# Kernel tuning notes

Hardware: AMD Instinct MI355X
Metric: run time of the kernel (lower is better)

Reference implementation:

```python
import jax, jax.numpy as jnp
import numpy as np

N_NODES = 50000
N_EDGES = 800000
IN_DIM = 128
HID = 128
BN_EPS = 1e-5


def _linear_init(key, fan_in, fan_out):
    kw, kb = jax.random.split(key)
    bound = 1.0 / np.sqrt(fan_in)
    w = jax.random.uniform(kw, (fan_in, fan_out), minval=-bound, maxval=bound, dtype=jnp.float32)
    b = jax.random.uniform(kb, (fan_out,), minval=-bound, maxval=bound, dtype=jnp.float32)
    return w, b


def setup_inputs() -> dict:
    key = jax.random.key(0)
    ks = jax.random.split(key, 8)
    x = jax.random.normal(ks[0], (N_NODES, IN_DIM), dtype=jnp.float32)
    edge_index = jax.random.randint(ks[1], (2, N_EDGES), 0, N_NODES, dtype=jnp.int32)
    # GIN layer 0 MLP: Linear(IN_DIM,HID) -> ReLU -> Linear(HID,HID)
    w0a, b0a = _linear_init(ks[2], IN_DIM, HID)
    w0b, b0b = _linear_init(ks[3], HID, HID)
    # GIN layer 1 MLP
    w1a, b1a = _linear_init(ks[4], HID, HID)
    w1b, b1b = _linear_init(ks[5], HID, HID)
    # encoder BatchNorm affine params (torch init: gamma=1, beta=0)
    bn_gamma = jnp.ones((HID,), jnp.float32)
    bn_beta = jnp.zeros((HID,), jnp.float32)
    # projection head: Linear(HID,HID) -> BatchNorm -> PReLU -> Dropout
    pw, pb = _linear_init(ks[6], HID, HID)
    pbn_gamma = jnp.ones((HID,), jnp.float32)
    pbn_beta = jnp.zeros((HID,), jnp.float32)
    prelu_a = jnp.asarray(0.25, jnp.float32)  # torch PReLU default init
    return {
        'x': x, 'edge_index': edge_index,
        'w0a': w0a, 'b0a': b0a, 'w0b': w0b, 'b0b': b0b,
        'w1a': w1a, 'b1a': b1a, 'w1b': w1b, 'b1b': b1b,
        'bn_gamma': bn_gamma, 'bn_beta': bn_beta,
        'pw': pw, 'pb': pb, 'pbn_gamma': pbn_gamma, 'pbn_beta': pbn_beta,
        'prelu_a': prelu_a,
    }


def _batch_norm(x, gamma, beta):
    # training-mode BatchNorm1d: biased variance over the node (batch) dim
    mu = jnp.mean(x, axis=0)
    var = jnp.var(x, axis=0)
    return gamma * (x - mu) * jax.lax.rsqrt(var + BN_EPS) + beta


def _gin_conv(z, src, dst, wa, ba, wb, bb):
    # sum-aggregate neighbor features: out[i] = (1+eps)*z[i] + sum_{j->i} z[j], eps=0
    agg = jax.ops.segment_sum(z[src], dst, num_segments=N_NODES)
    h = z + agg
    h = jax.nn.relu(h @ wa + ba)
    return h @ wb + bb


def reference(x, edge_index, w0a, b0a, w0b, b0b, w1a, b1a, w1b, b1b,
              bn_gamma, bn_beta, pw, pb, pbn_gamma, pbn_beta, prelu_a):
    src, dst = edge_index[0], edge_index[1]
    z = x
    z = jax.nn.relu(_gin_conv(z, src, dst, w0a, b0a, w0b, b0b))  # dropout: identity (deterministic)
    z = jax.nn.relu(_gin_conv(z, src, dst, w1a, b1a, w1b, b1b))
    z = _batch_norm(z, bn_gamma, bn_beta)
    p = z @ pw + pb
    p = _batch_norm(p, pbn_gamma, pbn_beta)
    p = jnp.where(p > 0, p, prelu_a * p)  # PReLU, single shared parameter
    return z, p
```

## Files before the change

kernel.cpp:

```cpp
#include <hip/hip_runtime.h>
#include <hip/hip_bf16.h>

#define NN 50000
#define NE 800000
#define HD 128
#define BN_EPS 1e-5f
#define MSTR 132
#define NBUK 782
#define PB 200
#define CHUNK 4000

typedef __attribute__((ext_vector_type(8))) __bf16 bf16x8;
typedef __attribute__((ext_vector_type(4))) __bf16 bf16x4;
typedef __attribute__((ext_vector_type(4))) float floatx4;

__global__ void k_zero_i(int* __restrict__ p, int n) {
    const int i = blockIdx.x * 256 + threadIdx.x;
    if (i < n) p[i] = 0;
}

__global__ __launch_bounds__(256) void k_cast(const float* __restrict__ X,
                                              __bf16* __restrict__ Y) {
    const int i8 = (blockIdx.x * 256 + threadIdx.x) * 8;
    const float4 a = *(const float4*)&X[i8];
    const float4 b = *(const float4*)&X[i8 + 4];
    bf16x8 o;
    o[0] = (__bf16)a.x; o[1] = (__bf16)a.y; o[2] = (__bf16)a.z; o[3] = (__bf16)a.w;
    o[4] = (__bf16)b.x; o[5] = (__bf16)b.y; o[6] = (__bf16)b.z; o[7] = (__bf16)b.w;
    *(bf16x8*)&Y[i8] = o;
}

__global__ void k_wprep(const float* __restrict__ W0, const float* __restrict__ W1,
                        const float* __restrict__ W2, const float* __restrict__ W3,
                        const float* __restrict__ W4,
                        __bf16* __restrict__ Bh, __bf16* __restrict__ Bl) {
    const int n = blockIdx.x, m = blockIdx.y, k = threadIdx.x;
    const float* W = (m == 0) ? W0 : (m == 1) ? W1 : (m == 2) ? W2 : (m == 3) ? W3 : W4;
    const float w = W[k * HD + n];
    const __bf16 h = (__bf16)w;
    const int ct = n >> 4, lm = n & 15;
    const int ks = k >> 5, lq = (k & 31) >> 3, j = k & 7;
    const int lane = lq * 16 + lm;
    const size_t o = (size_t)m * HD * HD + (size_t)(((ct * 4 + ks) * 64) + lane) * 8 + j;
    Bh[o] = h;
    Bl[o] = (__bf16)(w - (float)h);
}

__global__ __launch_bounds__(256) void k_bcount(const int* __restrict__ dst,
                                                int* __restrict__ gbtot) {
    __shared__ int h[NBUK];
    for (int i = threadIdx.x; i < NBUK; i += 256) h[i] = 0;
    __syncthreads();
    const int e0 = blockIdx.x * CHUNK;
    for (int i = threadIdx.x; i < CHUNK; i += 256)
        atomicAdd(&h[dst[e0 + i] >> 6], 1);
    __syncthreads();
    for (int i = threadIdx.x; i < NBUK; i += 256) {
        const int v = h[i];
        if (v) atomicAdd(&gbtot[i], v);
    }
}

__global__ __launch_bounds__(256) void k_bscan(const int* __restrict__ gbtot,
                                               int* __restrict__ bbase,
                                               int* __restrict__ gcur,
                                               int* __restrict__ rowptr) {
    __shared__ int sh[256];
    const int t = threadIdx.x;
    int v[4];
    int s = 0;
#pragma unroll
    for (int j = 0; j < 4; ++j) {
        const int idx = t * 4 + j;
        v[j] = (idx < NBUK) ? gbtot[idx] : 0;
        s += v[j];
    }
    sh[t] = s;
    __syncthreads();
#pragma unroll
    for (int st = 1; st < 256; st <<= 1) {
        int add = (t >= st) ? sh[t - st] : 0;
        __syncthreads();
        sh[t] += add;
        __syncthreads();
    }
    int run = sh[t] - s;
#pragma unroll
    for (int j = 0; j < 4; ++j) {
        const int idx = t * 4 + j;
        if (idx < NBUK) { bbase[idx] = run; gcur[idx] = run; }
        run += v[j];
    }
    if (t == 255) bbase[NBUK] = run;
    if (t == 0) rowptr[NN] = NE;
}

__global__ __launch_bounds__(256) void k_bscatter(const int* __restrict__ src,
                                                  const int* __restrict__ dst,
                                                  int* __restrict__ gcur,
                                                  int2* __restrict__ pairs) {
    __shared__ int h[NBUK];
    __shared__ int cur[NBUK];
    for (int i = threadIdx.x; i < NBUK; i += 256) h[i] = 0;
    __syncthreads();
    const int e0 = blockIdx.x * CHUNK;
    for (int i = threadIdx.x; i < CHUNK; i += 256)
        atomicAdd(&h[dst[e0 + i] >> 6], 1);
    __syncthreads();
    for (int i = threadIdx.x; i < NBUK; i += 256) {
        const int v = h[i];
        if (v) cur[i] = atomicAdd(&gcur[i], v);
    }
    __syncthreads();
    for (int i = threadIdx.x; i < CHUNK; i += 256) {
        const int d = dst[e0 + i];
        const int pos = atomicAdd(&cur[d >> 6], 1);
        pairs[pos] = make_int2(src[e0 + i], d);
    }
}

__global__ __launch_bounds__(256) void k_csrfin(const int2* __restrict__ pairs,
                                                const int* __restrict__ bbase,
                                                int* __restrict__ rowptr,
                                                int* __restrict__ esrc) {
    __shared__ int cnt[64], lof[64], cur[64];
    const int b = blockIdx.x;
    const int s = bbase[b], e = bbase[b + 1];
    const int tid = threadIdx.x;
    if (tid < 64) cnt[tid] = 0;
    __syncthreads();
    for (int i = s + tid; i < e; i += 256)
        atomicAdd(&cnt[pairs[i].y & 63], 1);
    __syncthreads();
    if (tid == 0) {
        int r = 0;
#pragma unroll
        for (int j = 0; j < 64; ++j) { lof[j] = r; cur[j] = r; r += cnt[j]; }
    }
    __syncthreads();
    if (tid < 64) {
        const int node = b * 64 + tid;
        if (node < NN) rowptr[node] = s + lof[tid];
    }
    for (int i = s + tid; i < e; i += 256) {
        const int2 p = pairs[i];
        const int pos = atomicAdd(&cur[p.y & 63], 1);
        esrc[s + pos] = p.x;
    }
}

__device__ __forceinline__ void split8(const float4 a, const float4 b,
                                       bf16x8& hi, bf16x8& lo) {
    hi[0] = (__bf16)a.x; lo[0] = (__bf16)(a.x - (float)hi[0]);
    hi[1] = (__bf16)a.y; lo[1] = (__bf16)(a.y - (float)hi[1]);
    hi[2] = (__bf16)a.z; lo[2] = (__bf16)(a.z - (float)hi[2]);
    hi[3] = (__bf16)a.w; lo[3] = (__bf16)(a.w - (float)hi[3]);
    hi[4] = (__bf16)b.x; lo[4] = (__bf16)(b.x - (float)hi[4]);
    hi[5] = (__bf16)b.y; lo[5] = (__bf16)(b.y - (float)hi[5]);
    hi[6] = (__bf16)b.z; lo[6] = (__bf16)(b.z - (float)hi[6]);
    hi[7] = (__bf16)b.w; lo[7] = (__bf16)(b.w - (float)hi[7]);
}

__device__ __forceinline__ void addb8(float4& a, float4& b, const bf16x8 v) {
    a.x += (float)v[0]; a.y += (float)v[1]; a.z += (float)v[2]; a.w += (float)v[3];
    b.x += (float)v[4]; b.y += (float)v[5]; b.z += (float)v[6]; b.w += (float)v[7];
}

__global__ __launch_bounds__(256) void k_aggb(const __bf16* __restrict__ Z,
                                              const int* __restrict__ rowptr,
                                              const int* __restrict__ esrc,
                                              float* __restrict__ H) {
    const int g = threadIdx.x >> 4;
    const int lg = threadIdx.x & 15;
    const int node = blockIdx.x * 16 + g;
    const int cb = lg * 8;
    const int start = rowptr[node], end = rowptr[node + 1];
    float4 a = {0.f, 0.f, 0.f, 0.f}, b = {0.f, 0.f, 0.f, 0.f};
    addb8(a, b, *(const bf16x8*)&Z[(size_t)node * HD + cb]);
    int k = start;
    for (; k + 8 <= end; k += 8) {
        const int s0 = esrc[k + 0], s1 = esrc[k + 1];
        const int s2 = esrc[k + 2], s3 = esrc[k + 3];
        const int s4 = esrc[k + 4], s5 = esrc[k + 5];
        const int s6 = esrc[k + 6], s7 = esrc[k + 7];
        const bf16x8 v0 = *(const bf16x8*)&Z[(size_t)s0 * HD + cb];
        const bf16x8 v1 = *(const bf16x8*)&Z[(size_t)s1 * HD + cb];
        const bf16x8 v2 = *(const bf16x8*)&Z[(size_t)s2 * HD + cb];
        const bf16x8 v3 = *(const bf16x8*)&Z[(size_t)s3 * HD + cb];
        const bf16x8 v4 = *(const bf16x8*)&Z[(size_t)s4 * HD + cb];
        const bf16x8 v5 = *(const bf16x8*)&Z[(size_t)s5 * HD + cb];
        const bf16x8 v6 = *(const bf16x8*)&Z[(size_t)s6 * HD + cb];
        const bf16x8 v7 = *(const bf16x8*)&Z[(size_t)s7 * HD + cb];
        addb8(a, b, v0); addb8(a, b, v1); addb8(a, b, v2); addb8(a, b, v3);
        addb8(a, b, v4); addb8(a, b, v5); addb8(a, b, v6); addb8(a, b, v7);
    }
    for (; k + 4 <= end; k += 4) {
        const int s0 = esrc[k + 0], s1 = esrc[k + 1];
        const int s2 = esrc[k + 2], s3 = esrc[k + 3];
        const bf16x8 v0 = *(const bf16x8*)&Z[(size_t)s0 * HD + cb];
        const bf16x8 v1 = *(const bf16x8*)&Z[(size_t)s1 * HD + cb];
        const bf16x8 v2 = *(const bf16x8*)&Z[(size_t)s2 * HD + cb];
        const bf16x8 v3 = *(const bf16x8*)&Z[(size_t)s3 * HD + cb];
        addb8(a, b, v0); addb8(a, b, v1); addb8(a, b, v2); addb8(a, b, v3);
    }
    for (; k < end; ++k) {
        const int s = esrc[k];
        addb8(a, b, *(const bf16x8*)&Z[(size_t)s * HD + cb]);
    }
    *(float4*)&H[(size_t)node * HD + cb] = a;
    *(float4*)&H[(size_t)node * HD + cb + 4] = b;
}

__device__ __forceinline__ void mfma_pass(floatx4 (&acc)[8], const bf16x8 ah,
                                          const bf16x8 al, const __bf16* Bh,
                                          const __bf16* Bl, int ks, int lane) {
#pragma unroll
    for (int ct = 0; ct < 8; ++ct) {
        const size_t bo = (size_t)(((ct * 4 + ks) * 64) + lane) * 8;
        const bf16x8 bh = *(const bf16x8*)&Bh[bo];
        const bf16x8 bl = *(const bf16x8*)&Bl[bo];
        acc[ct] = __builtin_amdgcn_mfma_f32_16x16x32_bf16(al, bh, acc[ct], 0, 0, 0);
        acc[ct] = __builtin_amdgcn_mfma_f32_16x16x32_bf16(ah, bl, acc[ct], 0, 0, 0);
        acc[ct] = __builtin_amdgcn_mfma_f32_16x16x32_bf16(ah, bh, acc[ct], 0, 0, 0);
    }
}

template <int STATS, int OUT16>
__global__ __launch_bounds__(256) void k_mlp(const float* __restrict__ A,
                                             const __bf16* __restrict__ Bh1,
                                             const __bf16* __restrict__ Bl1,
                                             const float* __restrict__ b1,
                                             const __bf16* __restrict__ Bh2,
                                             const __bf16* __restrict__ Bl2,
                                             const float* __restrict__ b2,
                                             float* __restrict__ C,
                                             __bf16* __restrict__ C16,
                                             float* __restrict__ pstat) {
    __shared__ float mid[4][16 * MSTR];
    __shared__ float ssum[128], ssq[128];
    const int tid = threadIdx.x;
    const int wid = tid >> 6, lane = tid & 63;
    const int lq = lane >> 4, lm = lane & 15;
    if (STATS) {
        if (tid < 128) { ssum[tid] = 0.f; ssq[tid] = 0.f; }
        __syncthreads();
    }
    const int rowbase = blockIdx.x * 64 + wid * 16;
    const int r0 = min(rowbase + lm, NN - 1);
    float* m = &mid[wid][0];

    floatx4 acc[8];
#pragma unroll
    for (int j = 0; j < 8; ++j) acc[j] = (floatx4){0.f, 0.f, 0.f, 0.f};
#pragma unroll
    for (int ks = 0; ks < 4; ++ks) {
        const int kk = ks * 32 + lq * 8;
        const float4 aa = *(const float4*)&A[(size_t)r0 * HD + kk];
        const float4 ab = *(const float4*)&A[(size_t)r0 * HD + kk + 4];
        bf16x8 ah, al;
        split8(aa, ab, ah, al);
        mfma_pass(acc, ah, al, Bh1, Bl1, ks, lane);
    }
#pragma unroll
    for (int ct = 0; ct < 8; ++ct) {
        const int col = ct * 16 + lm;
        const float bcol = b1[col];
#pragma unroll
        for (int r = 0; r < 4; ++r)
            m[(lq * 4 + r) * MSTR + col] = fmaxf(acc[ct][r] + bcol, 0.f);
    }
#pragma unroll
    for (int j = 0; j < 8; ++j) acc[j] = (floatx4){0.f, 0.f, 0.f, 0.f};
#pragma unroll
    for (int ks = 0; ks < 4; ++ks) {
        const int kk = ks * 32 + lq * 8;
        const float4 aa = *(const float4*)&m[lm * MSTR + kk];
        const float4 ab = *(const float4*)&m[lm * MSTR + kk + 4];
        bf16x8 ah, al;
        split8(aa, ab, ah, al);
        mfma_pass(acc, ah, al, Bh2, Bl2, ks, lane);
    }
#pragma unroll
    for (int ct = 0; ct < 8; ++ct) {
        const int col = ct * 16 + lm;
        const float bcol = b2[col];
#pragma unroll
        for (int r = 0; r < 4; ++r)
            m[(lq * 4 + r) * MSTR + col] = fmaxf(acc[ct][r] + bcol, 0.f);
    }
    float s0 = 0.f, s1 = 0.f, s2 = 0.f, s3 = 0.f;
    float q0 = 0.f, q1 = 0.f, q2 = 0.f, q3 = 0.f;
    const int c0 = (lane * 4) & 127;
#pragma unroll
    for (int p = 0; p < 8; ++p) {
        const int idx = p * 256 + lane * 4;
        const int r = idx >> 7;
        const float4 v = *(const float4*)&m[r * MSTR + c0];
        const int row = rowbase + r;
        if (row < NN) {
            if (OUT16) {
                bf16x4 o;
                o[0] = (__bf16)v.x; o[1] = (__bf16)v.y;
                o[2] = (__bf16)v.z; o[3] = (__bf16)v.w;
                *(bf16x4*)&C16[(size_t)row * HD + c0] = o;
            } else {
                *(float4*)&C[(size_t)row * HD + c0] = v;
            }
            if (STATS) {
                s0 += v.x; q0 = fmaf(v.x, v.x, q0);
                s1 += v.y; q1 = fmaf(v.y, v.y, q1);
                s2 += v.z; q2 = fmaf(v.z, v.z, q2);
                s3 += v.w; q3 = fmaf(v.w, v.w, q3);
            }
        }
    }
    if (STATS) {
        s0 += __shfl_xor(s0, 32); q0 += __shfl_xor(q0, 32);
        s1 += __shfl_xor(s1, 32); q1 += __shfl_xor(q1, 32);
        s2 += __shfl_xor(s2, 32); q2 += __shfl_xor(q2, 32);
        s3 += __shfl_xor(s3, 32); q3 += __shfl_xor(q3, 32);
        if (lane < 32) {
            atomicAdd(&ssum[c0 + 0], s0); atomicAdd(&ssq[c0 + 0], q0);
            atomicAdd(&ssum[c0 + 1], s1); atomicAdd(&ssq[c0 + 1], q1);
            atomicAdd(&ssum[c0 + 2], s2); atomicAdd(&ssq[c0 + 2], q2);
            atomicAdd(&ssum[c0 + 3], s3); atomicAdd(&ssq[c0 + 3], q3);
        }
        __syncthreads();
        if (tid < 128) {
            pstat[(size_t)blockIdx.x * 256 + tid] = ssum[tid];
            pstat[(size_t)blockIdx.x * 256 + 128 + tid] = ssq[tid];
        }
    }
}

__global__ __launch_bounds__(256) void k_proj(const float* __restrict__ Z2,
                                              const float* __restrict__ bnsc,
                                              const float* __restrict__ bnsh,
                                              float* __restrict__ Zout,
                                              const __bf16* __restrict__ Bh,
                                              const __bf16* __restrict__ Bl,
                                              const float* __restrict__ bias,
                                              float* __restrict__ C,
                                              float* __restrict__ pstat) {
    __shared__ float tb[4][16 * MSTR];
    __shared__ float ssum[128], ssq[128];
    const int tid = threadIdx.x;
    const int wid = tid >> 6, lane = tid & 63;
    const int lq = lane >> 4, lm = lane & 15;
    if (tid < 128) { ssum[tid] = 0.f; ssq[tid] = 0.f; }
    __syncthreads();
    const int rowbase = blockIdx.x * 64 + wid * 16;
    const int r0 = min(rowbase + lm, NN - 1);
    const bool rowok = (rowbase + lm) < NN;
    float* m = &tb[wid][0];

    floatx4 acc[8];
#pragma unroll
    for (int j = 0; j < 8; ++j) acc[j] = (floatx4){0.f, 0.f, 0.f, 0.f};
#pragma unroll
    for (int ks = 0; ks < 4; ++ks) {
        const int kk = ks * 32 + lq * 8;
        const float4 za = *(const float4*)&Z2[(size_t)r0 * HD + kk];
        const float4 zb = *(const float4*)&Z2[(size_t)r0 * HD + kk + 4];
        const float4 sca = *(const float4*)&bnsc[kk];
        const float4 scb = *(const float4*)&bnsc[kk + 4];
        const float4 sha = *(const float4*)&bnsh[kk];
        const float4 shb = *(const float4*)&bnsh[kk + 4];
        float4 aa, ab;
        aa.x = fmaf(za.x, sca.x, sha.x); aa.y = fmaf(za.y, sca.y, sha.y);
        aa.z = fmaf(za.z, sca.z, sha.z); aa.w = fmaf(za.w, sca.w, sha.w);
        ab.x = fmaf(zb.x, scb.x, shb.x); ab.y = fmaf(zb.y, scb.y, shb.y);
        ab.z = fmaf(zb.z, scb.z, shb.z); ab.w = fmaf(zb.w, scb.w, shb.w);
        if (rowok) {
            *(float4*)&Zout[(size_t)r0 * HD + kk] = aa;
            *(float4*)&Zout[(size_t)r0 * HD + kk + 4] = ab;
        }
        bf16x8 ah, al;
        split8(aa, ab, ah, al);
        mfma_pass(acc, ah, al, Bh, Bl, ks, lane);
    }
#pragma unroll
    for (int ct = 0; ct < 8; ++ct) {
        const int col = ct * 16 + lm;
        const float bcol = bias[col];
#pragma unroll
        for (int r = 0; r < 4; ++r)
            m[(lq * 4 + r) * MSTR + col] = acc[ct][r] + bcol;
    }
    float s0 = 0.f, s1 = 0.f, s2 = 0.f, s3 = 0.f;
    float q0 = 0.f, q1 = 0.f, q2 = 0.f, q3 = 0.f;
    const int c0 = (lane * 4) & 127;
#pragma unroll
    for (int p = 0; p < 8; ++p) {
        const int idx = p * 256 + lane * 4;
        const int r = idx >> 7;
        const float4 v = *(const float4*)&m[r * MSTR + c0];
        const int row = rowbase + r;
        if (row < NN) {
            *(float4*)&C[(size_t)row * HD + c0] = v;
            s0 += v.x; q0 = fmaf(v.x, v.x, q0);
            s1 += v.y; q1 = fmaf(v.y, v.y, q1);
            s2 += v.z; q2 = fmaf(v.z, v.z, q2);
            s3 += v.w; q3 = fmaf(v.w, v.w, q3);
        }
    }
    s0 += __shfl_xor(s0, 32); q0 += __shfl_xor(q0, 32);
    s1 += __shfl_xor(s1, 32); q1 += __shfl_xor(q1, 32);
    s2 += __shfl_xor(s2, 32); q2 += __shfl_xor(q2, 32);
    s3 += __shfl_xor(s3, 32); q3 += __shfl_xor(q3, 32);
    if (lane < 32) {
        atomicAdd(&ssum[c0 + 0], s0); atomicAdd(&ssq[c0 + 0], q0);
        atomicAdd(&ssum[c0 + 1], s1); atomicAdd(&ssq[c0 + 1], q1);
        atomicAdd(&ssum[c0 + 2], s2); atomicAdd(&ssq[c0 + 2], q2);
        atomicAdd(&ssum[c0 + 3], s3); atomicAdd(&ssq[c0 + 3], q3);
    }
    __syncthreads();
    if (tid < 128) {
        pstat[(size_t)blockIdx.x * 256 + tid] = ssum[tid];
        pstat[(size_t)blockIdx.x * 256 + 128 + tid] = ssq[tid];
    }
}

__global__ __launch_bounds__(256) void k_sred(const float* __restrict__ ps, int nblk,
                                              float* __restrict__ out) {
    const int j = threadIdx.x;
    float acc = 0.f;
    for (int r = blockIdx.x; r < nblk; r += 64)
        acc += ps[(size_t)r * 256 + j];
    out[blockIdx.x * 256 + j] = acc;
}

__global__ void k_bnfin(const float* __restrict__ pb2,
                        const float* __restrict__ gamma, const float* __restrict__ beta,
                        float* __restrict__ scale, float* __restrict__ shift) {
    const int c = threadIdx.x;
    float s = 0.f, q = 0.f;
    for (int b = 0; b < 64; ++b) {
        s += pb2[b * 256 + c];
        q += pb2[b * 256 + 128 + c];
    }
    const float mean = s * (1.f / NN);
    const float var = q * (1.f / NN) - mean * mean;
    const float sc = gamma[c] * rsqrtf(var + BN_EPS);
    scale[c] = sc;
    shift[c] = beta[c] - mean * sc;
}

__global__ void k_bnapply(const float* __restrict__ X, const float* __restrict__ scale,
                          const float* __restrict__ shift, float* __restrict__ Y,
                          const float* __restrict__ pa) {
    const int i4 = (blockIdx.x * 256 + threadIdx.x) * 4;
    const int c = i4 & 127;
    const float4 sc = *(const float4*)&scale[c];
    const float4 sh = *(const float4*)&shift[c];
    const float4 v = *(const float4*)&X[i4];
    float4 y;
    y.x = fmaf(v.x, sc.x, sh.x);
    y.y = fmaf(v.y, sc.y, sh.y);
    y.z = fmaf(v.z, sc.z, sh.z);
    y.w = fmaf(v.w, sc.w, sh.w);
    const float a = pa[0];
    if (y.x < 0.f) y.x *= a;
    if (y.y < 0.f) y.y *= a;
    if (y.z < 0.f) y.z *= a;
    if (y.w < 0.f) y.w *= a;
    *(float4*)&Y[i4] = y;
}

extern "C" void kernel_launch(void* const* d_in, const int* in_sizes, int n_in,
                              void* d_out, int out_size, void* d_ws, size_t ws_size,
                              hipStream_t stream) {
    const float* x = (const float*)d_in[0];
    const int* ei = (const int*)d_in[1];
    const float* w0a = (const float*)d_in[2];
    const float* b0a = (const float*)d_in[3];
    const float* w0b = (const float*)d_in[4];
    const float* b0b = (const float*)d_in[5];
    const float* w1a = (const float*)d_in[6];
    const float* b1a = (const float*)d_in[7];
    const float* w1b = (const float*)d_in[8];
    const float* b1b = (const float*)d_in[9];
    const float* bng = (const float*)d_in[10];
    const float* bnb = (const float*)d_in[11];
    const float* pw  = (const float*)d_in[12];
    const float* pb  = (const float*)d_in[13];
    const float* pbng = (const float*)d_in[14];
    const float* pbnb = (const float*)d_in[15];
    const float* pa = (const float*)d_in[16];

    float* outZ = (float*)d_out;
    float* outP = outZ + (size_t)NN * HD;

    float* ws = (float*)d_ws;
    float* bufH = ws;
    float* st = bufH + (size_t)NN * HD;
    int* rowptr = (int*)(st + 1024);
    int* esrc = rowptr + NN + 64;
    int* gbtot = esrc + NE;
    int* bbase = gbtot + 800;
    int* gcur = bbase + 800;
    __bf16* wth = (__bf16*)(gcur + 800);
    __bf16* wtl = wth + 5 * HD * HD;
    float* ps1 = (float*)(wtl + 5 * HD * HD);
    float* pb2a = ps1 + 800 * 256;
    float* ps2 = pb2a + 64 * 256;
    float* pb2b = ps2 + 800 * 256;

    __bf16* xb  = (__bf16*)bufH;
    __bf16* z1b = xb + (size_t)NN * HD;
    int2* pairs = (int2*)z1b;
    float* Hbuf = outP;

    const int* srcv = ei;
    const int* dstv = ei + NE;

    const int ELV = (NN * HD) / (256 * 4);
    const int CVB = (NN * HD) / (256 * 8);
    const int GB = (NN + 63) / 64;
    const int AB = NN / 16;

    k_wprep<<<dim3(HD, 5), HD, 0, stream>>>(w0a, w0b, w1a, w1b, pw, wth, wtl);
    k_cast<<<CVB, 256, 0, stream>>>(x, xb);
    k_zero_i<<<4, 256, 0, stream>>>(gbtot, 800);

    k_bcount<<<PB, 256, 0, stream>>>(dstv, gbtot);
    k_bscan<<<1, 256, 0, stream>>>(gbtot, bbase, gcur, rowptr);
    k_bscatter<<<PB, 256, 0, stream>>>(srcv, dstv, gcur, pairs);
    k_csrfin<<<NBUK, 256, 0, stream>>>(pairs, bbase, rowptr, esrc);

    k_aggb<<<AB, 256, 0, stream>>>(xb, rowptr, esrc, Hbuf);
    k_mlp<0, 1><<<GB, 256, 0, stream>>>(Hbuf,
                                        wth + 0 * HD * HD, wtl + 0 * HD * HD, b0a,
                                        wth + 1 * HD * HD, wtl + 1 * HD * HD, b0b,
                                        nullptr, z1b, nullptr);

    k_aggb<<<AB, 256, 0, stream>>>(z1b, rowptr, esrc, Hbuf);
    k_mlp<1, 0><<<GB, 256, 0, stream>>>(Hbuf,
                                        wth + 2 * HD * HD, wtl + 2 * HD * HD, b1a,
                                        wth + 3 * HD * HD, wtl + 3 * HD * HD, b1b,
                                        outP, nullptr, ps1);

    k_sred<<<64, 256, 0, stream>>>(ps1, GB, pb2a);
    k_bnfin<<<1, 128, 0, stream>>>(pb2a, bng, bnb, st + 256, st + 384);
    k_proj<<<GB, 256, 0, stream>>>(outP, st + 256, st + 384, outZ,
                                   wth + 4 * HD * HD, wtl + 4 * HD * HD, pb,
                                   outP, ps2);

    k_sred<<<64, 256, 0, stream>>>(ps2, GB, pb2b);
    k_bnfin<<<1, 128, 0, stream>>>(pb2b, pbng, pbnb, st + 768, st + 896);
    k_bnapply<<<ELV, 256, 0, stream>>>(outP, st + 768, st + 896, outP, pa);
}
```

Measured before the change: 329.3 us.

## Split MLP GEMM warps by output columns instead of rows to cut B-fragment reloads

In the MLP and projection kernels, each of the four waves used to own 16 rows and load all eight column tiles of the bf16 hi/lo weight fragments. Now each wave owns two column tiles across all 64 rows of the block, so each wave loads only a quarter of the weights while reading the A rows four times. A shared 64-row LDS tile with block-wide barriers replaces the per-wave scratch, because the second GEMM needs every column. This adds __syncthreads and repeated A-row loads per wave in exchange for less weight traffic and fewer B loads per MFMA.

Result: no change. 334.3 us (+1.5%).

```diff
diff --git a/kernel.cpp b/kernel.cpp
--- a/kernel.cpp
+++ b/kernel.cpp
@@ -211,18 +211,11 @@
     *(float4*)&H[(size_t)node * HD + cb + 4] = b;
 }
 
-__device__ __forceinline__ void mfma_pass(floatx4 (&acc)[8], const bf16x8 ah,
-                                          const bf16x8 al, const __bf16* Bh,
-                                          const __bf16* Bl, int ks, int lane) {
-#pragma unroll
-    for (int ct = 0; ct < 8; ++ct) {
-        const size_t bo = (size_t)(((ct * 4 + ks) * 64) + lane) * 8;
-        const bf16x8 bh = *(const bf16x8*)&Bh[bo];
-        const bf16x8 bl = *(const bf16x8*)&Bl[bo];
-        acc[ct] = __builtin_amdgcn_mfma_f32_16x16x32_bf16(al, bh, acc[ct], 0, 0, 0);
-        acc[ct] = __builtin_amdgcn_mfma_f32_16x16x32_bf16(ah, bl, acc[ct], 0, 0, 0);
-        acc[ct] = __builtin_amdgcn_mfma_f32_16x16x32_bf16(ah, bh, acc[ct], 0, 0, 0);
-    }
+__device__ __forceinline__ void mfma3(floatx4& acc, const bf16x8 ah, const bf16x8 al,
+                                      const bf16x8 bh, const bf16x8 bl) {
+    acc = __builtin_amdgcn_mfma_f32_16x16x32_bf16(al, bh, acc, 0, 0, 0);
+    acc = __builtin_amdgcn_mfma_f32_16x16x32_bf16(ah, bl, acc, 0, 0, 0);
+    acc = __builtin_amdgcn_mfma_f32_16x16x32_bf16(ah, bh, acc, 0, 0, 0);
 }
 
 template <int STATS, int OUT16>
@@ -236,66 +229,96 @@
                                              float* __restrict__ C,
                                              __bf16* __restrict__ C16,
                                              float* __restrict__ pstat) {
-    __shared__ float mid[4][16 * MSTR];
+    __shared__ float mid[64 * MSTR];
     __shared__ float ssum[128], ssq[128];
     const int tid = threadIdx.x;
     const int wid = tid >> 6, lane = tid & 63;
     const int lq = lane >> 4, lm = lane & 15;
     if (STATS) {
         if (tid < 128) { ssum[tid] = 0.f; ssq[tid] = 0.f; }
-        __syncthreads();
-    }
-    const int rowbase = blockIdx.x * 64 + wid * 16;
-    const int r0 = min(rowbase + lm, NN - 1);
-    float* m = &mid[wid][0];
-
-    floatx4 acc[8];
-#pragma unroll
-    for (int j = 0; j < 8; ++j) acc[j] = (floatx4){0.f, 0.f, 0.f, 0.f};
+    }
+    const int rowbase = blockIdx.x * 64;
+
+    floatx4 acc[4][2];
+#pragma unroll
+    for (int rg = 0; rg < 4; ++rg) {
+        acc[rg][0] = (floatx4){0.f, 0.f, 0.f, 0.f};
+        acc[rg][1] = (floatx4){0.f, 0.f, 0.f, 0.f};
+    }
 #pragma unroll
     for (int ks = 0; ks < 4; ++ks) {
         const int kk = ks * 32 + lq * 8;
-        const float4 aa = *(const float4*)&A[(size_t)r0 * HD + kk];
-        const float4 ab = *(const float4*)&A[(size_t)r0 * HD + kk + 4];
-        bf16x8 ah, al;
-        split8(aa, ab, ah, al);
-        mfma_pass(acc, ah, al, Bh1, Bl1, ks, lane);
-    }
-#pragma unroll
-    for (int ct = 0; ct < 8; ++ct) {
-        const int col = ct * 16 + lm;
+        const size_t bo0 = (size_t)((((wid * 2 + 0) * 4 + ks) * 64) + lane) * 8;
+        const size_t bo1 = (size_t)((((wid * 2 + 1) * 4 + ks) * 64) + lane) * 8;
+        const bf16x8 bh0 = *(const bf16x8*)&Bh1[bo0];
+        const bf16x8 bl0 = *(const bf16x8*)&Bl1[bo0];
+        const bf16x8 bh1v = *(const bf16x8*)&Bh1[bo1];
+        const bf16x8 bl1v = *(const bf16x8*)&Bl1[bo1];
+#pragma unroll
+        for (int rg = 0; rg < 4; ++rg) {
+            const int r0 = min(rowbase + rg * 16 + lm, NN - 1);
+            const float4 aa = *(const float4*)&A[(size_t)r0 * HD + kk];
+            const float4 ab = *(const float4*)&A[(size_t)r0 * HD + kk + 4];
+            bf16x8 ah, al;
+            split8(aa, ab, ah, al);
+            mfma3(acc[rg][0], ah, al, bh0, bl0);
+            mfma3(acc[rg][1], ah, al, bh1v, bl1v);
+        }
+    }
+#pragma unroll
+    for (int c4 = 0; c4 < 2; ++c4) {
+        const int col = (wid * 2 + c4) * 16 + lm;
         const float bcol = b1[col];
 #pragma unroll
-        for (int r = 0; r < 4; ++r)
-            m[(lq * 4 + r) * MSTR + col] = fmaxf(acc[ct][r] + bcol, 0.f);
-    }
-#pragma unroll
-    for (int j = 0; j < 8; ++j) acc[j] = (floatx4){0.f, 0.f, 0.f, 0.f};
+        for (int rg = 0; rg < 4; ++rg)
+#pragma unroll
+            for (int r = 0; r < 4; ++r)
+                mid[(rg * 16 + lq * 4 + r) * MSTR + col] = fmaxf(acc[rg][c4][r] + bcol, 0.f);
+    }
+    __syncthreads();
+#pragma unroll
+    for (int rg = 0; rg < 4; ++rg) {
+        acc[rg][0] = (floatx4){0.f, 0.f, 0.f, 0.f};
+        acc[rg][1] = (floatx4){0.f, 0.f, 0.f, 0.f};
+    }
 #pragma unroll
     for (int ks = 0; ks < 4; ++ks) {
         const int kk = ks * 32 + lq * 8;
-        const float4 aa = *(const float4*)&m[lm * MSTR + kk];
-        const float4 ab = *(const float4*)&m[lm * MSTR + kk + 4];
-        bf16x8 ah, al;
-        split8(aa, ab, ah, al);
-        mfma_pass(acc, ah, al, Bh2, Bl2, ks, lane);
-    }
-#pragma unroll
-    for (int ct = 0; ct < 8; ++ct) {
-        const int col = ct * 16 + lm;
+        const size_t bo0 = (size_t)((((wid * 2 + 0) * 4 + ks) * 64) + lane) * 8;
+        const size_t bo1 = (size_t)((((wid * 2 + 1) * 4 + ks) * 64) + lane) * 8;
+        const bf16x8 bh0 = *(const bf16x8*)&Bh2[bo0];
+        const bf16x8 bl0 = *(const bf16x8*)&Bl2[bo0];
+        const bf16x8 bh1v = *(const bf16x8*)&Bh2[bo1];
+        const bf16x8 bl1v = *(const bf16x8*)&Bl2[bo1];
+#pragma unroll
+        for (int rg = 0; rg < 4; ++rg) {
+            const float4 aa = *(const float4*)&mid[(rg * 16 + lm) * MSTR + kk];
+            const float4 ab = *(const float4*)&mid[(rg * 16 + lm) * MSTR + kk + 4];
+            bf16x8 ah, al;
+            split8(aa, ab, ah, al);
+            mfma3(acc[rg][0], ah, al, bh0, bl0);
+            mfma3(acc[rg][1], ah, al, bh1v, bl1v);
+        }
+    }
+    __syncthreads();
+#pragma unroll
+    for (int c4 = 0; c4 < 2; ++c4) {
+        const int col = (wid * 2 + c4) * 16 + lm;
         const float bcol = b2[col];
 #pragma unroll
-        for (int r = 0; r < 4; ++r)
-            m[(lq * 4 + r) * MSTR + col] = fmaxf(acc[ct][r] + bcol, 0.f);
-    }
+        for (int rg = 0; rg < 4; ++rg)
+#pragma unroll
+            for (int r = 0; r < 4; ++r)
+                mid[(rg * 16 + lq * 4 + r) * MSTR + col] = fmaxf(acc[rg][c4][r] + bcol, 0.f);
+    }
+    __syncthreads();
     float s0 = 0.f, s1 = 0.f, s2 = 0.f, s3 = 0.f;
     float q0 = 0.f, q1 = 0.f, q2 = 0.f, q3 = 0.f;
-    const int c0 = (lane * 4) & 127;
+    const int c0 = (tid * 4) & 127;
 #pragma unroll
     for (int p = 0; p < 8; ++p) {
-        const int idx = p * 256 + lane * 4;
-        const int r = idx >> 7;
-        const float4 v = *(const float4*)&m[r * MSTR + c0];
+        const int r = p * 8 + (tid >> 5);
+        const float4 v = *(const float4*)&mid[r * MSTR + c0];
         const int row = rowbase + r;
         if (row < NN) {
             if (OUT16) {
@@ -342,59 +365,72 @@
                                               const float* __restrict__ bias,
                                               float* __restrict__ C,
                                               float* __restrict__ pstat) {
-    __shared__ float tb[4][16 * MSTR];
+    __shared__ float mid[64 * MSTR];
     __shared__ float ssum[128], ssq[128];
     const int tid = threadIdx.x;
     const int wid = tid >> 6, lane = tid & 63;
     const int lq = lane >> 4, lm = lane & 15;
     if (tid < 128) { ssum[tid] = 0.f; ssq[tid] = 0.f; }
-    __syncthreads();
-    const int rowbase = blockIdx.x * 64 + wid * 16;
-    const int r0 = min(rowbase + lm, NN - 1);
-    const bool rowok = (rowbase + lm) < NN;
-    float* m = &tb[wid][0];
-
-    floatx4 acc[8];
-#pragma unroll
-    for (int j = 0; j < 8; ++j) acc[j] = (floatx4){0.f, 0.f, 0.f, 0.f};
+    const int rowbase = blockIdx.x * 64;
+
+    floatx4 acc[4][2];
+#pragma unroll
+    for (int rg = 0; rg < 4; ++rg) {
+        acc[rg][0] = (floatx4){0.f, 0.f, 0.f, 0.f};
+        acc[rg][1] = (floatx4){0.f, 0.f, 0.f, 0.f};
+    }
 #pragma unroll
     for (int ks = 0; ks < 4; ++ks) {
         const int kk = ks * 32 + lq * 8;
-        const float4 za = *(const float4*)&Z2[(size_t)r0 * HD + kk];
-        const float4 zb = *(const float4*)&Z2[(size_t)r0 * HD + kk + 4];
+        const size_t bo0 = (size_t)((((wid * 2 + 0) * 4 + ks) * 64) + lane) * 8;
+        const size_t bo1 = (size_t)((((wid * 2 + 1) * 4 + ks) * 64) + lane) * 8;
+        const bf16x8 bh0 = *(const bf16x8*)&Bh[bo0];
+        const bf16x8 bl0 = *(const bf16x8*)&Bl[bo0];
+        const bf16x8 bh1v = *(const bf16x8*)&Bh[bo1];
+        const bf16x8 bl1v = *(const bf16x8*)&Bl[bo1];
         const float4 sca = *(const float4*)&bnsc[kk];
         const float4 scb = *(const float4*)&bnsc[kk + 4];
         const float4 sha = *(const float4*)&bnsh[kk];
         const float4 shb = *(const float4*)&bnsh[kk + 4];
-        float4 aa, ab;
-        aa.x = fmaf(za.x, sca.x, sha.x); aa.y = fmaf(za.y, sca.y, sha.y);
-        aa.z = fmaf(za.z, sca.z, sha.z); aa.w = fmaf(za.w, sca.w, sha.w);
-        ab.x = fmaf(zb.x, scb.x, shb.x); ab.y = fmaf(zb.y, scb.y, shb.y);
-        ab.z = fmaf(zb.z, scb.z, shb.z); ab.w = fmaf(zb.w, scb.w, shb.w);
-        if (rowok) {
-            *(float4*)&Zout[(size_t)r0 * HD + kk] = aa;
-            *(float4*)&Zout[(size_t)r0 * HD + kk + 4] = ab;
-        }
-        bf16x8 ah, al;
-        split8(aa, ab, ah, al);
-        mfma_pass(acc, ah, al, Bh, Bl, ks, lane);
-    }
-#pragma unroll
-    for (int ct = 0; ct < 8; ++ct) {
-        const int col = ct * 16 + lm;
+#pragma unroll
+        for (int rg = 0; rg < 4; ++rg) {
+            const int rglob = rowbase + rg * 16 + lm;
+            const int r0 = min(rglob, NN - 1);
+            const float4 za = *(const float4*)&Z2[(size_t)r0 * HD + kk];
+            const float4 zb = *(const float4*)&Z2[(size_t)r0 * HD + kk + 4];
+            float4 aa, ab;
+            aa.x = fmaf(za.x, sca.x, sha.x); aa.y = fmaf(za.y, sca.y, sha.y);
+            aa.z = fmaf(za.z, sca.z, sha.z); aa.w = fmaf(za.w, sca.w, sha.w);
+            ab.x = fmaf(zb.x, scb.x, shb.x); ab.y = fmaf(zb.y, scb.y, shb.y);
+            ab.z = fmaf(zb.z, scb.z, shb.z); ab.w = fmaf(zb.w, scb.w, shb.w);
+            if (wid == 0 && rglob < NN) {
+                *(float4*)&Zout[(size_t)r0 * HD + kk] = aa;
+                *(float4*)&Zout[(size_t)r0 * HD + kk + 4] = ab;
+            }
+            bf16x8 ah, al;
+            split8(aa, ab, ah, al);
+            mfma3(acc[rg][0], ah, al, bh0, bl0);
+            mfma3(acc[rg][1], ah, al, bh1v, bl1v);
+        }
+    }
+#pragma unroll
+    for (int c4 = 0; c4 < 2; ++c4) {
+        const int col = (wid * 2 + c4) * 16 + lm;
         const float bcol = bias[col];
 #pragma unroll
-        for (int r = 0; r < 4; ++r)
-            m[(lq * 4 + r) * MSTR + col] = acc[ct][r] + bcol;
-    }
+        for (int rg = 0; rg < 4; ++rg)
+#pragma unroll
+            for (int r = 0; r < 4; ++r)
+                mid[(rg * 16 + lq * 4 + r) * MSTR + col] = acc[rg][c4][r] + bcol;
+    }
+    __syncthreads();
     float s0 = 0.f, s1 = 0.f, s2 = 0.f, s3 = 0.f;
     float q0 = 0.f, q1 = 0.f, q2 = 0.f, q3 = 0.f;
-    const int c0 = (lane * 4) & 127;
+    const int c0 = (tid * 4) & 127;
 #pragma unroll
     for (int p = 0; p < 8; ++p) {
-        const int idx = p * 256 + lane * 4;
-        const int r = idx >> 7;
-        const float4 v = *(const float4*)&m[r * MSTR + c0];
+        const int r = p * 8 + (tid >> 5);
+        const float4 v = *(const float4*)&mid[r * MSTR + c0];
         const int row = rowbase + r;
         if (row < NN) {
             *(float4*)&C[(size_t)row * HD + c0] = v;
```
